# Kernel optimization log

Measured on AMD Instinct MI355X. Metric: run time of the kernel, lower is better.

Reference implementation:

```python
import jax, jax.numpy as jnp
import numpy as np

N_NODES = 100000
N_EDGES = 3200000
HID = 52
N_LAYERS = 3


def setup_inputs() -> dict:
    key = jax.random.key(0)
    ks = jax.random.split(key, 6)
    x = jax.random.normal(ks[0], (N_NODES, HID), dtype=jnp.float32)
    edge_index = jax.random.randint(ks[1], (2, N_EDGES), 0, N_NODES, dtype=jnp.int32)
    w1 = jax.random.normal(ks[2], (N_LAYERS, HID, 2 * HID), dtype=jnp.float32) * 0.1
    b1 = jnp.zeros((N_LAYERS, 2 * HID), dtype=jnp.float32)
    w2 = jax.random.normal(ks[3], (N_LAYERS, 2 * HID, HID), dtype=jnp.float32) * 0.1
    b2 = jnp.zeros((N_LAYERS, HID), dtype=jnp.float32)
    eps = jnp.zeros((N_LAYERS,), dtype=jnp.float32)
    lin_w = jax.random.normal(ks[4], (HID * (N_LAYERS + 1), HID), dtype=jnp.float32) * 0.1
    lin_b = jnp.zeros((HID,), dtype=jnp.float32)
    return {"x": x, "edge_index": edge_index, "w1": w1, "b1": b1,
            "w2": w2, "b2": b2, "eps": eps, "lin_w": lin_w, "lin_b": lin_b}


def reference(x, edge_index, w1, b1, w2, b2, eps, lin_w, lin_b):
    src, dst = edge_index[0], edge_index[1]
    n = x.shape[0]
    h = x
    h_list = [x]
    for l in range(N_LAYERS):
        # GINConv: sum-aggregate neighbor features at target nodes
        agg = jax.ops.segment_sum(h[src], dst, num_segments=n)  # [N, HID]
        z = (1.0 + eps[l]) * h + agg
        # 2-layer MLP: Linear -> ReLU -> Linear
        z = jnp.maximum(z @ w1[l] + b1[l], 0.0) @ w2[l] + b2[l]
        # outer ReLU (dropout p=0 is identity)
        h = jnp.maximum(z, 0.0)
        h_list.append(h)
    node_repr = jnp.concatenate(h_list, axis=1)  # [N, HID*(L+1)]
    return node_repr @ lin_w + lin_b
```

## Files before the change

kernel.cpp:

```cpp
#include <hip/hip_runtime.h>

#define HID 52
#define HID2 104
#define P1_CHUNK 8192
#define NBIN_MAX 512

typedef unsigned short ushort_t;
typedef unsigned int uint_t;
typedef short bf16x8 __attribute__((ext_vector_type(8)));
typedef float f32x4 __attribute__((ext_vector_type(4)));
typedef float f32x2 __attribute__((ext_vector_type(2)));

__device__ __forceinline__ ushort_t f2bf(float f) {
    union { float f; uint_t u; } c; c.f = f;
    uint_t u = c.u + 0x7FFFu + ((c.u >> 16) & 1u);
    return (ushort_t)(u >> 16);
}
__device__ __forceinline__ float bflo(uint_t u) {
    union { uint_t u; float f; } c; c.u = u << 16; return c.f;
}
__device__ __forceinline__ float bfhi(uint_t u) {
    union { uint_t u; float f; } c; c.u = u & 0xFFFF0000u; return c.f;
}
__device__ __forceinline__ f32x2 unpk(uint_t u) {
    return (f32x2){bflo(u), bfhi(u)};
}


__global__ __launch_bounds__(256) void bhist_kernel(const int* __restrict__ dst,
                                                    int* __restrict__ ghist, int E) {
    __shared__ int lh[NBIN_MAX];
    int tid = threadIdx.x;
    lh[tid] = 0; lh[tid + 256] = 0;
    __syncthreads();
    int base = blockIdx.x * P1_CHUNK;
    int cend = min(P1_CHUNK, E - base);
    for (int i = tid; i < cend; i += 256) atomicAdd(&lh[dst[base + i] >> 8], 1);
    __syncthreads();
    int c = lh[tid];       if (c) atomicAdd(&ghist[tid], c);
    c = lh[tid + 256];     if (c) atomicAdd(&ghist[tid + 256], c);
}

__global__ __launch_bounds__(256) void bscan_kernel(const int* __restrict__ ghist,
                                                    int* __restrict__ binstart,
                                                    int* __restrict__ gcur,
                                                    int NBIN, int E) {
    __shared__ int c[NBIN_MAX];
    __shared__ int ps[256];
    int tid = threadIdx.x;
    int b0 = 2 * tid, b1 = 2 * tid + 1;
    c[b0] = ghist[b0]; c[b1] = ghist[b1];
    __syncthreads();
    int pair = c[b0] + c[b1];
    ps[tid] = pair;
    __syncthreads();
    for (int off = 1; off < 256; off <<= 1) {
        int t = (tid >= off) ? ps[tid - off] : 0;
        __syncthreads();
        ps[tid] += t;
        __syncthreads();
    }
    int ex = ps[tid] - pair;
    binstart[b0] = ex;        gcur[b0] = ex;
    binstart[b1] = ex + c[b0]; gcur[b1] = ex + c[b0];
    if (tid == 0) binstart[NBIN] = E;
}

__global__ __launch_bounds__(256) void pass1_kernel(const int* __restrict__ src,
                                                    const int* __restrict__ dst,
                                                    int* __restrict__ gcur,
                                                    uint_t* __restrict__ packed, int E) {
    __shared__ uint_t stage[P1_CHUNK];
    __shared__ ushort_t sbin[P1_CHUNK];
    __shared__ int cnt[NBIN_MAX];
    __shared__ int sst[NBIN_MAX];
    __shared__ int curs[NBIN_MAX];
    __shared__ int gbase[NBIN_MAX];
    __shared__ int ps[256];
    int tid = threadIdx.x;
    int base = blockIdx.x * P1_CHUNK;
    int cend = min(P1_CHUNK, E - base);
    cnt[tid] = 0; cnt[tid + 256] = 0;
    __syncthreads();
    for (int i = tid; i < cend; i += 256) atomicAdd(&cnt[dst[base + i] >> 8], 1);
    __syncthreads();
    int b0 = 2 * tid, b1 = 2 * tid + 1;
    int c0 = cnt[b0], c1 = cnt[b1];
    int pair = c0 + c1;
    ps[tid] = pair;
    __syncthreads();
    for (int off = 1; off < 256; off <<= 1) {
        int t = (tid >= off) ? ps[tid - off] : 0;
        __syncthreads();
        ps[tid] += t;
        __syncthreads();
    }
    int ex = ps[tid] - pair;
    sst[b0] = ex;       curs[b0] = ex;
    sst[b1] = ex + c0;  curs[b1] = ex + c0;
    gbase[b0] = c0 ? atomicAdd(&gcur[b0], c0) : 0;
    gbase[b1] = c1 ? atomicAdd(&gcur[b1], c1) : 0;
    __syncthreads();
    for (int i = tid; i < cend; i += 256) {
        int d = dst[base + i];
        int s = src[base + i];
        int b = d >> 8;
        int pos = atomicAdd(&curs[b], 1);
        stage[pos] = ((uint_t)s << 8) | (uint_t)(d & 255);
        sbin[pos] = (ushort_t)b;
    }
    __syncthreads();
    for (int i = tid; i < cend; i += 256) {
        int b = sbin[i];
        packed[gbase[b] + (i - sst[b])] = stage[i];
    }
}

__global__ __launch_bounds__(256) void pass2_kernel(const uint_t* __restrict__ packed,
                                                    const int* __restrict__ binstart,
                                                    int* __restrict__ srcsorted,
                                                    int* __restrict__ nrs,
                                                    int* __restrict__ ndeg, int N) {
    __shared__ int ncnt[256];
    __shared__ int ps[256];
    __shared__ int curs[256];
    int b = blockIdx.x;
    int beg = binstart[b], end = binstart[b + 1];
    int obase = beg + b * 4096;
    int tid = threadIdx.x;
    ncnt[tid] = 0;
    __syncthreads();
    for (int i = beg + tid; i < end; i += 256) atomicAdd(&ncnt[packed[i] & 255u], 1);
    __syncthreads();
    int v = ncnt[tid];
    int pv = (v + 15) & ~15;
    ps[tid] = pv;
    __syncthreads();
    for (int off = 1; off < 256; off <<= 1) {
        int t = (tid >= off) ? ps[tid - off] : 0;
        __syncthreads();
        ps[tid] += t;
        __syncthreads();
    }
    int start = obase + ps[tid] - pv;
    int node = b * 256 + tid;
    if (node < N) { nrs[node] = start; ndeg[node] = pv; }
    curs[tid] = start;
    __syncthreads();
    for (int i = beg + tid; i < end; i += 256) {
        uint_t p = packed[i];
        int pos = atomicAdd(&curs[p & 255u], 1);
        srcsorted[pos] = (int)(p >> 8);
    }
    __syncthreads();
    for (int i = start + v; i < start + pv; i++) srcsorted[i] = N;
}

__global__ __launch_bounds__(256) void setup_kernel(const float* __restrict__ x,
                                                    const float* __restrict__ w1,
                                                    const float* __restrict__ w2,
                                                    const float* __restrict__ lin_w,
                                                    ushort_t* __restrict__ xb,
                                                    ushort_t* __restrict__ h1b,
                                                    ushort_t* __restrict__ h2b,
                                                    ushort_t* __restrict__ h3b,
                                                    ushort_t* __restrict__ w1f,
                                                    ushort_t* __restrict__ w2f,
                                                    ushort_t* __restrict__ linf,
                                                    int* __restrict__ ghist,
                                                    int n, int nxblk) {
    int blk = blockIdx.x;
    int tid = threadIdx.x;
    if (blk < nxblk) {
        int t = blk * 256 + tid;
        if (t >= n * 16) return;
        int node = t >> 4, pp = t & 15;
        int c0 = pp * 4;
        ushort_t o[4];
#pragma unroll
        for (int j = 0; j < 4; j++) {
            int c = c0 + j;
            o[j] = (c < HID) ? f2bf(x[(size_t)node * HID + c]) : 0;
        }
        uint_t u0 = (uint_t)o[0] | ((uint_t)o[1] << 16);
        uint_t u1 = (uint_t)o[2] | ((uint_t)o[3] << 16);
        *(uint2*)(xb + (size_t)node * 64 + c0) = make_uint2(u0, u1);
        return;
    }
    if (blk == nxblk) {
        ushort_t* arr = (tid < 64) ? xb : (tid < 128) ? h1b : (tid < 192) ? h2b : h3b;
        arr[(size_t)n * 64 + (tid & 63)] = 0;
        ghist[tid] = 0; ghist[tid + 256] = 0;
        return;
    }
    int gid = (blk - nxblk - 1) * 4 + (tid >> 6);
    int lane = tid & 63;
    if (gid >= 122) return;
    int m = lane & 15, q = lane >> 4;
    ushort_t o[8];
    ushort_t* dstp;
    if (gid < 42) {
        int l = gid / 14, r = gid % 14, ct = r >> 1, ks = r & 1;
        int nn = ct * 16 + m;
#pragma unroll
        for (int j = 0; j < 8; j++) {
            int k = ks * 32 + q * 8 + j;
            o[j] = (k < HID && nn < HID2) ? f2bf(w1[((size_t)l * HID + k) * HID2 + nn]) : 0;
        }
        dstp = w1f + ((size_t)(l * 14 + ct * 2 + ks) * 64 + lane) * 8;
    } else if (gid < 90) {
        int g2 = gid - 42, l = g2 / 16, r = g2 % 16, ct = r >> 2, ks = r & 3;
        int nn = ct * 16 + m;
#pragma unroll
        for (int j = 0; j < 8; j++) {
            int k = ks * 32 + q * 8 + j;
            o[j] = (k < HID2 && nn < HID) ? f2bf(w2[((size_t)l * HID2 + k) * HID + nn]) : 0;
        }
        dstp = w2f + ((size_t)(l * 16 + ct * 4 + ks) * 64 + lane) * 8;
    } else {
        int g2 = gid - 90, ct = g2 >> 3, ks = g2 & 7;
        int nn = ct * 16 + m;
#pragma unroll
        for (int j = 0; j < 8; j++) {
            int kg = ks * 32 + q * 8 + j;
            int seg = kg >> 6, kk = kg & 63;
            o[j] = (kk < HID && nn < HID) ? f2bf(lin_w[((size_t)seg * HID + kk) * HID + nn]) : 0;
        }
        dstp = linf + ((size_t)(ct * 8 + ks) * 64 + lane) * 8;
    }
    uint4 u;
    u.x = (uint_t)o[0] | ((uint_t)o[1] << 16);
    u.y = (uint_t)o[2] | ((uint_t)o[3] << 16);
    u.z = (uint_t)o[4] | ((uint_t)o[5] << 16);
    u.w = (uint_t)o[6] | ((uint_t)o[7] << 16);
    *(uint4*)dstp = u;
}

__global__ __launch_bounds__(256) void agg_kernel(const ushort_t* __restrict__ hb,
                                                  const int* __restrict__ nrs,
                                                  const int* __restrict__ ndeg,
                                                  const int* __restrict__ srcsorted,
                                                  const float* __restrict__ eps,
                                                  ushort_t* __restrict__ zb, int n) {
    int wid = (blockIdx.x * blockDim.x + threadIdx.x) >> 6;
    if (wid >= n) return;
    int lane = threadIdx.x & 63;
    int g = lane >> 3, sub = lane & 7;
    int beg = nrs[wid];
    int total = ndeg[wid];
    const ushort_t* hsub = hb + sub * 8;
    const int* ss = srcsorted + beg + g;

    f32x2 A0 = {0,0}, A1 = {0,0}, A2 = {0,0}, A3 = {0,0};
    f32x2 B0 = {0,0}, B1 = {0,0}, B2 = {0,0}, B3 = {0,0};
    if (total > 0) {
        int f0 = ss[0], f1 = ss[8], f2r = ss[16], f3r = ss[24];
        for (int b = 0; b < total; b += 32) {
            bool ok = (b + 16) < total;
            int e0 = f0, e1 = f1;
            int e2 = ok ? f2r : n;
            int e3 = ok ? f3r : n;
            f0 = ss[b + 32]; f1 = ss[b + 40]; f2r = ss[b + 48]; f3r = ss[b + 56];
            uint4 v0 = *(const uint4*)(hsub + (size_t)e0 * 64);
            uint4 v1 = *(const uint4*)(hsub + (size_t)e1 * 64);
            uint4 v2 = *(const uint4*)(hsub + (size_t)e2 * 64);
            uint4 v3 = *(const uint4*)(hsub + (size_t)e3 * 64);
            A0 += unpk(v0.x); A1 += unpk(v0.y); A2 += unpk(v0.z); A3 += unpk(v0.w);
            B0 += unpk(v1.x); B1 += unpk(v1.y); B2 += unpk(v1.z); B3 += unpk(v1.w);
            A0 += unpk(v2.x); A1 += unpk(v2.y); A2 += unpk(v2.z); A3 += unpk(v2.w);
            B0 += unpk(v3.x); B1 += unpk(v3.y); B2 += unpk(v3.z); B3 += unpk(v3.w);
        }
    }
    A0 += B0; A1 += B1; A2 += B2; A3 += B3;
    float a0 = A0.x, a1 = A0.y, a2 = A1.x, a3 = A1.y;
    float a4 = A2.x, a5 = A2.y, a6 = A3.x, a7 = A3.y;
#pragma unroll
    for (int msk = 8; msk <= 32; msk <<= 1) {
        a0 += __shfl_xor(a0, msk); a1 += __shfl_xor(a1, msk);
        a2 += __shfl_xor(a2, msk); a3 += __shfl_xor(a3, msk);
        a4 += __shfl_xor(a4, msk); a5 += __shfl_xor(a5, msk);
        a6 += __shfl_xor(a6, msk); a7 += __shfl_xor(a7, msk);
    }
    if (lane < 8) {
        float sc = 1.0f + eps[0];
        uint4 sv = *(const uint4*)(hb + (size_t)wid * 64 + lane * 8);
        float o0 = fmaf(sc, bflo(sv.x), a0), o1 = fmaf(sc, bfhi(sv.x), a1);
        float o2 = fmaf(sc, bflo(sv.y), a2), o3 = fmaf(sc, bfhi(sv.y), a3);
        float o4 = fmaf(sc, bflo(sv.z), a4), o5 = fmaf(sc, bfhi(sv.z), a5);
        float o6 = fmaf(sc, bflo(sv.w), a6), o7 = fmaf(sc, bfhi(sv.w), a7);
        uint4 u;
        u.x = (uint_t)f2bf(o0) | ((uint_t)f2bf(o1) << 16);
        u.y = (uint_t)f2bf(o2) | ((uint_t)f2bf(o3) << 16);
        u.z = (uint_t)f2bf(o4) | ((uint_t)f2bf(o5) << 16);
        u.w = (uint_t)f2bf(o6) | ((uint_t)f2bf(o7) << 16);
        *(uint4*)(zb + (size_t)wid * 64 + lane * 8) = u;
    }
}

#define HSTRIDE 136
__global__ __launch_bounds__(256) void mlp_kernel(const ushort_t* __restrict__ zb,
                                                  const ushort_t* __restrict__ w1f,
                                                  const float* __restrict__ b1,
                                                  const ushort_t* __restrict__ w2f,
                                                  const float* __restrict__ b2,
                                                  ushort_t* __restrict__ hbout, int n) {
    __shared__ ushort_t hid[64 * HSTRIDE];
    int tid = threadIdx.x;
    int w = tid >> 6, lane = tid & 63, m = lane & 15, q = lane >> 4;
    for (int i = tid; i < 64 * 32; i += 256) {
        int r = i >> 5, c = HID2 + (i & 31);
        hid[r * HSTRIDE + c] = 0;
    }
    __syncthreads();

    int nb = blockIdx.x * 64 + w * 16;
    f32x4 acc1[7];
#pragma unroll
    for (int ct = 0; ct < 7; ct++) {
        int col = ct * 16 + m;
        float bv = (col < HID2) ? b1[col] : 0.f;
        acc1[ct] = (f32x4){bv, bv, bv, bv};
    }
    int anode = min(nb + m, n - 1);
#pragma unroll
    for (int ks = 0; ks < 2; ks++) {
        bf16x8 a = *(const bf16x8*)(zb + (size_t)anode * 64 + ks * 32 + q * 8);
#pragma unroll
        for (int ct = 0; ct < 7; ct++) {
            bf16x8 b = *(const bf16x8*)(w1f + ((size_t)(ct * 2 + ks) * 64 + lane) * 8);
            acc1[ct] = __builtin_amdgcn_mfma_f32_16x16x32_bf16(a, b, acc1[ct], 0, 0, 0);
        }
    }
#pragma unroll
    for (int ct = 0; ct < 7; ct++) {
#pragma unroll
        for (int r = 0; r < 4; r++) {
            float v = fmaxf(acc1[ct][r], 0.f);
            int row = w * 16 + q * 4 + r;
            hid[row * HSTRIDE + ct * 16 + m] = f2bf(v);
        }
    }
    f32x4 acc2[4];
#pragma unroll
    for (int ct = 0; ct < 4; ct++) {
        int col = ct * 16 + m;
        float bv = (col < HID) ? b2[col] : 0.f;
        acc2[ct] = (f32x4){bv, bv, bv, bv};
    }
#pragma unroll
    for (int ks = 0; ks < 4; ks++) {
        bf16x8 a = *(const bf16x8*)&hid[(w * 16 + m) * HSTRIDE + ks * 32 + q * 8];
#pragma unroll
        for (int ct = 0; ct < 4; ct++) {
            bf16x8 b = *(const bf16x8*)(w2f + ((size_t)(ct * 4 + ks) * 64 + lane) * 8);
            acc2[ct] = __builtin_amdgcn_mfma_f32_16x16x32_bf16(a, b, acc2[ct], 0, 0, 0);
        }
    }
#pragma unroll
    for (int ct = 0; ct < 4; ct++) {
#pragma unroll
        for (int r = 0; r < 4; r++) {
            int node = nb + q * 4 + r;
            if (node < n) {
                float v = fmaxf(acc2[ct][r], 0.f);
                hbout[(size_t)node * 64 + ct * 16 + m] = f2bf(v);
            }
        }
    }
}

__global__ __launch_bounds__(256) void final_kernel(const ushort_t* __restrict__ xb,
                                                    const ushort_t* __restrict__ h1b,
                                                    const ushort_t* __restrict__ h2b,
                                                    const ushort_t* __restrict__ h3b,
                                                    const ushort_t* __restrict__ linf,
                                                    const float* __restrict__ lin_b,
                                                    float* __restrict__ out, int ntiles) {
    int tid = threadIdx.x;
    int w = tid >> 6, lane = tid & 63, m = lane & 15, q = lane >> 4;
    int tile = blockIdx.x * 4 + w;
    if (tile >= ntiles) return;
    int nb = tile * 16;
    const ushort_t* segs[4] = {xb, h1b, h2b, h3b};
    f32x4 acc[4];
#pragma unroll
    for (int ct = 0; ct < 4; ct++) {
        int col = ct * 16 + m;
        float bv = (col < HID) ? lin_b[col] : 0.f;
        acc[ct] = (f32x4){bv, bv, bv, bv};
    }
#pragma unroll
    for (int ks = 0; ks < 8; ks++) {
        const ushort_t* p = segs[ks >> 1];
        bf16x8 a = *(const bf16x8*)(p + (size_t)(nb + m) * 64 + (ks & 1) * 32 + q * 8);
#pragma unroll
        for (int ct = 0; ct < 4; ct++) {
            bf16x8 b = *(const bf16x8*)(linf + ((size_t)(ct * 8 + ks) * 64 + lane) * 8);
            acc[ct] = __builtin_amdgcn_mfma_f32_16x16x32_bf16(a, b, acc[ct], 0, 0, 0);
        }
    }
#pragma unroll
    for (int ct = 0; ct < 4; ct++) {
        int col = ct * 16 + m;
        if (col < HID) {
#pragma unroll
            for (int r = 0; r < 4; r++)
                out[(size_t)(nb + q * 4 + r) * HID + col] = acc[ct][r];
        }
    }
}

extern "C" void kernel_launch(void* const* d_in, const int* in_sizes, int n_in,
                              void* d_out, int out_size, void* d_ws, size_t ws_size,
                              hipStream_t stream) {
    const float* x     = (const float*)d_in[0];
    const int*   ei    = (const int*)d_in[1];
    const float* w1    = (const float*)d_in[2];
    const float* b1    = (const float*)d_in[3];
    const float* w2    = (const float*)d_in[4];
    const float* b2    = (const float*)d_in[5];
    const float* eps   = (const float*)d_in[6];
    const float* lin_w = (const float*)d_in[7];
    const float* lin_b = (const float*)d_in[8];
    float* out = (float*)d_out;

    const int N = in_sizes[0] / HID;
    const int E = in_sizes[1] / 2;
    const int* src = ei;
    const int* dst = ei + E;

    const int NBIN = (N + 255) / 256;

    char* p = (char*)d_ws;
    const size_t ROWS = (size_t)(N + 1) * 64 * 2;
    ushort_t* xb  = (ushort_t*)p;  p += ROWS;
    ushort_t* zb  = (ushort_t*)p;  p += ROWS;
    ushort_t* h1b = (ushort_t*)p;  p += ROWS;
    ushort_t* h2b = (ushort_t*)p;  p += ROWS;
    ushort_t* h3b = (ushort_t*)p;  p += ROWS;
    ushort_t* w1f = (ushort_t*)p;  p += 3 * 14 * 512 * 2;
    ushort_t* w2f = (ushort_t*)p;  p += 3 * 16 * 512 * 2;
    ushort_t* linf= (ushort_t*)p;  p += 32 * 512 * 2;
    int* ghist    = (int*)p;       p += 528 * 4;
    int* binstart = (int*)p;       p += 528 * 4;
    int* gcur     = (int*)p;       p += 528 * 4;
    int* nrs      = (int*)p;       p += (size_t)(N + 4) * 4;
    int* ndeg     = (int*)p;       p += (size_t)(N + 4) * 4;
    uint_t* packed = (uint_t*)p;   p += (size_t)E * 4;
    int* srcsorted = (int*)p;

    ushort_t* hbs[4] = {xb, h1b, h2b, h3b};

    const int BLK = 256;
    const int NP1 = (E + P1_CHUNK - 1) / P1_CHUNK;
    const int NXBLK = (N * 16 + BLK - 1) / BLK;
    dim3 blk(BLK);
    dim3 grid_agg(((size_t)N * 64 + BLK - 1) / BLK);

    setup_kernel<<<NXBLK + 1 + 31, blk, 0, stream>>>(x, w1, w2, lin_w,
                                                     xb, h1b, h2b, h3b,
                                                     w1f, w2f, linf, ghist, N, NXBLK);
    bhist_kernel<<<NP1, blk, 0, stream>>>(dst, ghist, E);
    bscan_kernel<<<1, blk, 0, stream>>>(ghist, binstart, gcur, NBIN, E);
    pass1_kernel<<<NP1, blk, 0, stream>>>(src, dst, gcur, packed, E);
    pass2_kernel<<<NBIN, blk, 0, stream>>>(packed, binstart, srcsorted, nrs, ndeg, N);

    const int NBUCK = (N + 63) / 64;
    for (int l = 0; l < 3; l++) {
        agg_kernel<<<grid_agg, blk, 0, stream>>>(hbs[l], nrs, ndeg, srcsorted, eps + l, zb, N);
        mlp_kernel<<<NBUCK, blk, 0, stream>>>(zb,
                                              w1f + (size_t)l * 14 * 512,
                                              b1 + (size_t)l * HID2,
                                              w2f + (size_t)l * 16 * 512,
                                              b2 + (size_t)l * HID,
                                              hbs[l + 1], N);
    }
    final_kernel<<<(6250 + 3) / 4 + 1, blk, 0, stream>>>(xb, h1b, h2b, h3b, linf, lin_b,
                                                         out, (N + 15) / 16);
}
```

Baseline: 403.8 us.

## Fuse neighbor aggregation, MLP, and final projection into one per-layer kernel

Aggregation for each 64-node tile now runs inside the MLP kernel, and the z tile is kept in shared memory instead of going through a global zb buffer. The last layer also fuses the final linear projection, so h3 stays in shared memory. This removes a global round trip of intermediates and four kernel launches. In exchange, each wave now aggregates 16 nodes one after another, which lowers per-node parallelism for the latency-bound gather and raises shared memory use per block, which may reduce occupancy.

```diff
diff --git a/kernel.cpp b/kernel.cpp
--- a/kernel.cpp
+++ b/kernel.cpp
@@ -4,6 +4,7 @@
 #define HID2 104
 #define P1_CHUNK 8192
 #define NBIN_MAX 512
+#define HSTRIDE 136
 
 typedef unsigned short ushort_t;
 typedef unsigned int uint_t;
@@ -163,7 +164,6 @@
                                                     ushort_t* __restrict__ xb,
                                                     ushort_t* __restrict__ h1b,
                                                     ushort_t* __restrict__ h2b,
-                                                    ushort_t* __restrict__ h3b,
                                                     ushort_t* __restrict__ w1f,
                                                     ushort_t* __restrict__ w2f,
                                                     ushort_t* __restrict__ linf,
@@ -188,7 +188,7 @@
         return;
     }
     if (blk == nxblk) {
-        ushort_t* arr = (tid < 64) ? xb : (tid < 128) ? h1b : (tid < 192) ? h2b : h3b;
+        ushort_t* arr = (tid < 64) ? xb : (tid < 128) ? h1b : h2b;
         arr[(size_t)n * 64 + (tid & 63)] = 0;
         ghist[tid] = 0; ghist[tid + 256] = 0;
         return;
@@ -236,84 +236,88 @@
     *(uint4*)dstp = u;
 }
 
-__global__ __launch_bounds__(256) void agg_kernel(const ushort_t* __restrict__ hb,
-                                                  const int* __restrict__ nrs,
-                                                  const int* __restrict__ ndeg,
-                                                  const int* __restrict__ srcsorted,
-                                                  const float* __restrict__ eps,
-                                                  ushort_t* __restrict__ zb, int n) {
-    int wid = (blockIdx.x * blockDim.x + threadIdx.x) >> 6;
-    if (wid >= n) return;
-    int lane = threadIdx.x & 63;
+template<int LAST>
+__global__ __launch_bounds__(256) void layer_kernel(
+        const ushort_t* __restrict__ hbin,
+        const int* __restrict__ nrs, const int* __restrict__ ndeg,
+        const int* __restrict__ srcsorted,
+        const float* __restrict__ eps,
+        const ushort_t* __restrict__ w1f, const float* __restrict__ b1,
+        const ushort_t* __restrict__ w2f, const float* __restrict__ b2,
+        ushort_t* __restrict__ hbout,
+        const ushort_t* __restrict__ xb, const ushort_t* __restrict__ h1b,
+        const ushort_t* __restrict__ linf, const float* __restrict__ lin_b,
+        float* __restrict__ out, int n) {
+    __shared__ uint4 zt[64 * 9];
+    __shared__ ushort_t hid[64 * HSTRIDE];
+    __shared__ ushort_t h3t[LAST ? 64 * 68 : 1];
+
+    int tid = threadIdx.x;
+    int w = tid >> 6, lane = tid & 63;
     int g = lane >> 3, sub = lane & 7;
-    int beg = nrs[wid];
-    int total = ndeg[wid];
-    const ushort_t* hsub = hb + sub * 8;
-    const int* ss = srcsorted + beg + g;
-
-    f32x2 A0 = {0,0}, A1 = {0,0}, A2 = {0,0}, A3 = {0,0};
-    f32x2 B0 = {0,0}, B1 = {0,0}, B2 = {0,0}, B3 = {0,0};
-    if (total > 0) {
-        int f0 = ss[0], f1 = ss[8], f2r = ss[16], f3r = ss[24];
-        for (int b = 0; b < total; b += 32) {
-            bool ok = (b + 16) < total;
-            int e0 = f0, e1 = f1;
-            int e2 = ok ? f2r : n;
-            int e3 = ok ? f3r : n;
-            f0 = ss[b + 32]; f1 = ss[b + 40]; f2r = ss[b + 48]; f3r = ss[b + 56];
-            uint4 v0 = *(const uint4*)(hsub + (size_t)e0 * 64);
-            uint4 v1 = *(const uint4*)(hsub + (size_t)e1 * 64);
-            uint4 v2 = *(const uint4*)(hsub + (size_t)e2 * 64);
-            uint4 v3 = *(const uint4*)(hsub + (size_t)e3 * 64);
-            A0 += unpk(v0.x); A1 += unpk(v0.y); A2 += unpk(v0.z); A3 += unpk(v0.w);
-            B0 += unpk(v1.x); B1 += unpk(v1.y); B2 += unpk(v1.z); B3 += unpk(v1.w);
-            A0 += unpk(v2.x); A1 += unpk(v2.y); A2 += unpk(v2.z); A3 += unpk(v2.w);
-            B0 += unpk(v3.x); B1 += unpk(v3.y); B2 += unpk(v3.z); B3 += unpk(v3.w);
-        }
-    }
-    A0 += B0; A1 += B1; A2 += B2; A3 += B3;
-    float a0 = A0.x, a1 = A0.y, a2 = A1.x, a3 = A1.y;
-    float a4 = A2.x, a5 = A2.y, a6 = A3.x, a7 = A3.y;
-#pragma unroll
-    for (int msk = 8; msk <= 32; msk <<= 1) {
-        a0 += __shfl_xor(a0, msk); a1 += __shfl_xor(a1, msk);
-        a2 += __shfl_xor(a2, msk); a3 += __shfl_xor(a3, msk);
-        a4 += __shfl_xor(a4, msk); a5 += __shfl_xor(a5, msk);
-        a6 += __shfl_xor(a6, msk); a7 += __shfl_xor(a7, msk);
-    }
-    if (lane < 8) {
-        float sc = 1.0f + eps[0];
-        uint4 sv = *(const uint4*)(hb + (size_t)wid * 64 + lane * 8);
-        float o0 = fmaf(sc, bflo(sv.x), a0), o1 = fmaf(sc, bfhi(sv.x), a1);
-        float o2 = fmaf(sc, bflo(sv.y), a2), o3 = fmaf(sc, bfhi(sv.y), a3);
-        float o4 = fmaf(sc, bflo(sv.z), a4), o5 = fmaf(sc, bfhi(sv.z), a5);
-        float o6 = fmaf(sc, bflo(sv.w), a6), o7 = fmaf(sc, bfhi(sv.w), a7);
-        uint4 u;
-        u.x = (uint_t)f2bf(o0) | ((uint_t)f2bf(o1) << 16);
-        u.y = (uint_t)f2bf(o2) | ((uint_t)f2bf(o3) << 16);
-        u.z = (uint_t)f2bf(o4) | ((uint_t)f2bf(o5) << 16);
-        u.w = (uint_t)f2bf(o6) | ((uint_t)f2bf(o7) << 16);
-        *(uint4*)(zb + (size_t)wid * 64 + lane * 8) = u;
-    }
-}
-
-#define HSTRIDE 136
-__global__ __launch_bounds__(256) void mlp_kernel(const ushort_t* __restrict__ zb,
-                                                  const ushort_t* __restrict__ w1f,
-                                                  const float* __restrict__ b1,
-                                                  const ushort_t* __restrict__ w2f,
-                                                  const float* __restrict__ b2,
-                                                  ushort_t* __restrict__ hbout, int n) {
-    __shared__ ushort_t hid[64 * HSTRIDE];
-    int tid = threadIdx.x;
-    int w = tid >> 6, lane = tid & 63, m = lane & 15, q = lane >> 4;
+    int m = lane & 15, q = lane >> 4;
+    int nb = blockIdx.x * 64;
+
     for (int i = tid; i < 64 * 32; i += 256) {
         int r = i >> 5, c = HID2 + (i & 31);
         hid[r * HSTRIDE + c] = 0;
     }
-    __syncthreads();
-
-    int nb = blockIdx.x * 64 + w * 16;
+
+    float sc = 1.0f + eps[0];
+    for (int i = 0; i < 16; i++) {
+        int node = nb + w * 16 + i;
+        int nc = min(node, n - 1);
+        int beg = nrs[nc];
+        int total = ndeg[nc];
+        const ushort_t* hsub = hbin + sub * 8;
+        const int* ss = srcsorted + beg + g;
+
+        f32x2 A0 = {0,0}, A1 = {0,0}, A2 = {0,0}, A3 = {0,0};
+        f32x2 B0 = {0,0}, B1 = {0,0}, B2 = {0,0}, B3 = {0,0};
+        if (total > 0) {
+            int f0 = ss[0], f1 = ss[8], f2r = ss[16], f3r = ss[24];
+            for (int b = 0; b < total; b += 32) {
+                bool ok = (b + 16) < total;
+                int e0 = f0, e1 = f1;
+                int e2 = ok ? f2r : n;
+                int e3 = ok ? f3r : n;
+                f0 = ss[b + 32]; f1 = ss[b + 40]; f2r = ss[b + 48]; f3r = ss[b + 56];
+                uint4 v0 = *(const uint4*)(hsub + (size_t)e0 * 64);
+                uint4 v1 = *(const uint4*)(hsub + (size_t)e1 * 64);
+                uint4 v2 = *(const uint4*)(hsub + (size_t)e2 * 64);
+                uint4 v3 = *(const uint4*)(hsub + (size_t)e3 * 64);
+                A0 += unpk(v0.x); A1 += unpk(v0.y); A2 += unpk(v0.z); A3 += unpk(v0.w);
+                B0 += unpk(v1.x); B1 += unpk(v1.y); B2 += unpk(v1.z); B3 += unpk(v1.w);
+                A0 += unpk(v2.x); A1 += unpk(v2.y); A2 += unpk(v2.z); A3 += unpk(v2.w);
+                B0 += unpk(v3.x); B1 += unpk(v3.y); B2 += unpk(v3.z); B3 += unpk(v3.w);
+            }
+        }
+        A0 += B0; A1 += B1; A2 += B2; A3 += B3;
+        float a0 = A0.x, a1 = A0.y, a2 = A1.x, a3 = A1.y;
+        float a4 = A2.x, a5 = A2.y, a6 = A3.x, a7 = A3.y;
+#pragma unroll
+        for (int msk = 8; msk <= 32; msk <<= 1) {
+            a0 += __shfl_xor(a0, msk); a1 += __shfl_xor(a1, msk);
+            a2 += __shfl_xor(a2, msk); a3 += __shfl_xor(a3, msk);
+            a4 += __shfl_xor(a4, msk); a5 += __shfl_xor(a5, msk);
+            a6 += __shfl_xor(a6, msk); a7 += __shfl_xor(a7, msk);
+        }
+        if (lane < 8) {
+            uint4 sv = *(const uint4*)(hbin + (size_t)nc * 64 + lane * 8);
+            float o0 = fmaf(sc, bflo(sv.x), a0), o1 = fmaf(sc, bfhi(sv.x), a1);
+            float o2 = fmaf(sc, bflo(sv.y), a2), o3 = fmaf(sc, bfhi(sv.y), a3);
+            float o4 = fmaf(sc, bflo(sv.z), a4), o5 = fmaf(sc, bfhi(sv.z), a5);
+            float o6 = fmaf(sc, bflo(sv.w), a6), o7 = fmaf(sc, bfhi(sv.w), a7);
+            uint4 u;
+            u.x = (uint_t)f2bf(o0) | ((uint_t)f2bf(o1) << 16);
+            u.y = (uint_t)f2bf(o2) | ((uint_t)f2bf(o3) << 16);
+            u.z = (uint_t)f2bf(o4) | ((uint_t)f2bf(o5) << 16);
+            u.w = (uint_t)f2bf(o6) | ((uint_t)f2bf(o7) << 16);
+            zt[(w * 16 + i) * 9 + lane] = u;
+        }
+    }
+    __syncthreads();
+
     f32x4 acc1[7];
 #pragma unroll
     for (int ct = 0; ct < 7; ct++) {
@@ -321,10 +325,9 @@
         float bv = (col < HID2) ? b1[col] : 0.f;
         acc1[ct] = (f32x4){bv, bv, bv, bv};
     }
-    int anode = min(nb + m, n - 1);
 #pragma unroll
     for (int ks = 0; ks < 2; ks++) {
-        bf16x8 a = *(const bf16x8*)(zb + (size_t)anode * 64 + ks * 32 + q * 8);
+        bf16x8 a = *(const bf16x8*)&zt[(w * 16 + m) * 9 + ks * 4 + q];
 #pragma unroll
         for (int ct = 0; ct < 7; ct++) {
             bf16x8 b = *(const bf16x8*)(w1f + ((size_t)(ct * 2 + ks) * 64 + lane) * 8);
@@ -356,56 +359,63 @@
             acc2[ct] = __builtin_amdgcn_mfma_f32_16x16x32_bf16(a, b, acc2[ct], 0, 0, 0);
         }
     }
-#pragma unroll
-    for (int ct = 0; ct < 4; ct++) {
-#pragma unroll
-        for (int r = 0; r < 4; r++) {
-            int node = nb + q * 4 + r;
-            if (node < n) {
+
+    if (!LAST) {
+#pragma unroll
+        for (int ct = 0; ct < 4; ct++) {
+#pragma unroll
+            for (int r = 0; r < 4; r++) {
+                int node = nb + w * 16 + q * 4 + r;
+                if (node < n) {
+                    float v = fmaxf(acc2[ct][r], 0.f);
+                    hbout[(size_t)node * 64 + ct * 16 + m] = f2bf(v);
+                }
+            }
+        }
+    } else {
+#pragma unroll
+        for (int ct = 0; ct < 4; ct++) {
+#pragma unroll
+            for (int r = 0; r < 4; r++) {
                 float v = fmaxf(acc2[ct][r], 0.f);
-                hbout[(size_t)node * 64 + ct * 16 + m] = f2bf(v);
-            }
-        }
-    }
-}
-
-__global__ __launch_bounds__(256) void final_kernel(const ushort_t* __restrict__ xb,
-                                                    const ushort_t* __restrict__ h1b,
-                                                    const ushort_t* __restrict__ h2b,
-                                                    const ushort_t* __restrict__ h3b,
-                                                    const ushort_t* __restrict__ linf,
-                                                    const float* __restrict__ lin_b,
-                                                    float* __restrict__ out, int ntiles) {
-    int tid = threadIdx.x;
-    int w = tid >> 6, lane = tid & 63, m = lane & 15, q = lane >> 4;
-    int tile = blockIdx.x * 4 + w;
-    if (tile >= ntiles) return;
-    int nb = tile * 16;
-    const ushort_t* segs[4] = {xb, h1b, h2b, h3b};
-    f32x4 acc[4];
-#pragma unroll
-    for (int ct = 0; ct < 4; ct++) {
-        int col = ct * 16 + m;
-        float bv = (col < HID) ? lin_b[col] : 0.f;
-        acc[ct] = (f32x4){bv, bv, bv, bv};
-    }
-#pragma unroll
-    for (int ks = 0; ks < 8; ks++) {
-        const ushort_t* p = segs[ks >> 1];
-        bf16x8 a = *(const bf16x8*)(p + (size_t)(nb + m) * 64 + (ks & 1) * 32 + q * 8);
+                h3t[(w * 16 + q * 4 + r) * 68 + ct * 16 + m] = f2bf(v);
+            }
+        }
+        f32x4 accF[4];
 #pragma unroll
         for (int ct = 0; ct < 4; ct++) {
-            bf16x8 b = *(const bf16x8*)(linf + ((size_t)(ct * 8 + ks) * 64 + lane) * 8);
-            acc[ct] = __builtin_amdgcn_mfma_f32_16x16x32_bf16(a, b, acc[ct], 0, 0, 0);
-        }
-    }
-#pragma unroll
-    for (int ct = 0; ct < 4; ct++) {
-        int col = ct * 16 + m;
-        if (col < HID) {
-#pragma unroll
-            for (int r = 0; r < 4; r++)
-                out[(size_t)(nb + q * 4 + r) * HID + col] = acc[ct][r];
+            int col = ct * 16 + m;
+            float bv = (col < HID) ? lin_b[col] : 0.f;
+            accF[ct] = (f32x4){bv, bv, bv, bv};
+        }
+        int nodeA = min(nb + w * 16 + m, n - 1);
+        const ushort_t* segs[3] = {xb, h1b, hbin};
+#pragma unroll
+        for (int ks = 0; ks < 8; ks++) {
+            bf16x8 a;
+            if (ks < 6) {
+                const ushort_t* p = segs[ks >> 1];
+                a = *(const bf16x8*)(p + (size_t)nodeA * 64 + (ks & 1) * 32 + q * 8);
+            } else {
+                a = *(const bf16x8*)&h3t[(w * 16 + m) * 68 + (ks & 1) * 32 + q * 8];
+            }
+#pragma unroll
+            for (int ct = 0; ct < 4; ct++) {
+                bf16x8 b = *(const bf16x8*)(linf + ((size_t)(ct * 8 + ks) * 64 + lane) * 8);
+                accF[ct] = __builtin_amdgcn_mfma_f32_16x16x32_bf16(a, b, accF[ct], 0, 0, 0);
+            }
+        }
+#pragma unroll
+        for (int ct = 0; ct < 4; ct++) {
+            int col = ct * 16 + m;
+            if (col < HID) {
+#pragma unroll
+                for (int r = 0; r < 4; r++) {
+                    int node = nb + w * 16 + q * 4 + r;
+                    if (node < n)
+                        out[(size_t)node * HID + col] = accF[ct][r];
+                }
+            }
         }
     }
 }
@@ -434,10 +444,8 @@
     char* p = (char*)d_ws;
     const size_t ROWS = (size_t)(N + 1) * 64 * 2;
     ushort_t* xb  = (ushort_t*)p;  p += ROWS;
-    ushort_t* zb  = (ushort_t*)p;  p += ROWS;
     ushort_t* h1b = (ushort_t*)p;  p += ROWS;
     ushort_t* h2b = (ushort_t*)p;  p += ROWS;
-    ushort_t* h3b = (ushort_t*)p;  p += ROWS;
     ushort_t* w1f = (ushort_t*)p;  p += 3 * 14 * 512 * 2;
     ushort_t* w2f = (ushort_t*)p;  p += 3 * 16 * 512 * 2;
     ushort_t* linf= (ushort_t*)p;  p += 32 * 512 * 2;
@@ -449,32 +457,33 @@
     uint_t* packed = (uint_t*)p;   p += (size_t)E * 4;
     int* srcsorted = (int*)p;
 
-    ushort_t* hbs[4] = {xb, h1b, h2b, h3b};
-
     const int BLK = 256;
     const int NP1 = (E + P1_CHUNK - 1) / P1_CHUNK;
     const int NXBLK = (N * 16 + BLK - 1) / BLK;
+    const int NBUCK = (N + 63) / 64;
     dim3 blk(BLK);
-    dim3 grid_agg(((size_t)N * 64 + BLK - 1) / BLK);
 
     setup_kernel<<<NXBLK + 1 + 31, blk, 0, stream>>>(x, w1, w2, lin_w,
-                                                     xb, h1b, h2b, h3b,
+                                                     xb, h1b, h2b,
                                                      w1f, w2f, linf, ghist, N, NXBLK);
     bhist_kernel<<<NP1, blk, 0, stream>>>(dst, ghist, E);
     bscan_kernel<<<1, blk, 0, stream>>>(ghist, binstart, gcur, NBIN, E);
     pass1_kernel<<<NP1, blk, 0, stream>>>(src, dst, gcur, packed, E);
     pass2_kernel<<<NBIN, blk, 0, stream>>>(packed, binstart, srcsorted, nrs, ndeg, N);
 
-    const int NBUCK = (N + 63) / 64;
-    for (int l = 0; l < 3; l++) {
-        agg_kernel<<<grid_agg, blk, 0, stream>>>(hbs[l], nrs, ndeg, srcsorted, eps + l, zb, N);
-        mlp_kernel<<<NBUCK, blk, 0, stream>>>(zb,
-                                              w1f + (size_t)l * 14 * 512,
-                                              b1 + (size_t)l * HID2,
-                                              w2f + (size_t)l * 16 * 512,
-                                              b2 + (size_t)l * HID,
-                                              hbs[l + 1], N);
-    }
-    final_kernel<<<(6250 + 3) / 4 + 1, blk, 0, stream>>>(xb, h1b, h2b, h3b, linf, lin_b,
-                                                         out, (N + 15) / 16);
-}
+    layer_kernel<0><<<NBUCK, blk, 0, stream>>>(xb, nrs, ndeg, srcsorted, eps + 0,
+                                               w1f + 0 * 14 * 512, b1 + 0 * HID2,
+                                               w2f + 0 * 16 * 512, b2 + 0 * HID,
+                                               h1b, nullptr, nullptr, nullptr, nullptr,
+                                               nullptr, N);
+    layer_kernel<0><<<NBUCK, blk, 0, stream>>>(h1b, nrs, ndeg, srcsorted, eps + 1,
+                                               w1f + 1 * 14 * 512, b1 + 1 * HID2,
+                                               w2f + 1 * 16 * 512, b2 + 1 * HID,
+                                               h2b, nullptr, nullptr, nullptr, nullptr,
+                                               nullptr, N);
+    layer_kernel<1><<<NBUCK, blk, 0, stream>>>(h2b, nrs, ndeg, srcsorted, eps + 2,
+                                               w1f + 2 * 14 * 512, b1 + 2 * HID2,
+                                               w2f + 2 * 16 * 512, b2 + 2 * HID,
+                                               nullptr, xb, h1b,
+                                               linf, lin_b, out, N);
+}
```

Result: slower. 464.7 us (+15.1%).

## Fuse bin histogram into setup kernel and drop separate scan kernel

Applied to the files above, without the earlier changes.

The destination-bin histogram moves into extra blocks of the setup kernel, and the standalone scan kernel is removed. pass1 and pass2 now each recompute the bin prefix sum from the global histogram, and a memset zeroes the counters. pass2 also sub-sorts each node's edge list by the high bit of the source index, so gathers in the aggregation kernel get some locality. This trades two kernel launches for redundant per-block scans, and it adds a larger shared-memory histogram in pass2.

```diff
diff --git a/kernel.cpp b/kernel.cpp
--- a/kernel.cpp
+++ b/kernel.cpp
@@ -4,6 +4,7 @@
 #define HID2 104
 #define P1_CHUNK 8192
 #define NBIN_MAX 512
+#define HSTRIDE 136
 
 typedef unsigned short ushort_t;
 typedef unsigned int uint_t;
@@ -26,140 +27,11 @@
     return (f32x2){bflo(u), bfhi(u)};
 }
 
-
-__global__ __launch_bounds__(256) void bhist_kernel(const int* __restrict__ dst,
-                                                    int* __restrict__ ghist, int E) {
-    __shared__ int lh[NBIN_MAX];
-    int tid = threadIdx.x;
-    lh[tid] = 0; lh[tid + 256] = 0;
-    __syncthreads();
-    int base = blockIdx.x * P1_CHUNK;
-    int cend = min(P1_CHUNK, E - base);
-    for (int i = tid; i < cend; i += 256) atomicAdd(&lh[dst[base + i] >> 8], 1);
-    __syncthreads();
-    int c = lh[tid];       if (c) atomicAdd(&ghist[tid], c);
-    c = lh[tid + 256];     if (c) atomicAdd(&ghist[tid + 256], c);
-}
-
-__global__ __launch_bounds__(256) void bscan_kernel(const int* __restrict__ ghist,
-                                                    int* __restrict__ binstart,
-                                                    int* __restrict__ gcur,
-                                                    int NBIN, int E) {
-    __shared__ int c[NBIN_MAX];
-    __shared__ int ps[256];
-    int tid = threadIdx.x;
-    int b0 = 2 * tid, b1 = 2 * tid + 1;
-    c[b0] = ghist[b0]; c[b1] = ghist[b1];
-    __syncthreads();
-    int pair = c[b0] + c[b1];
-    ps[tid] = pair;
-    __syncthreads();
-    for (int off = 1; off < 256; off <<= 1) {
-        int t = (tid >= off) ? ps[tid - off] : 0;
-        __syncthreads();
-        ps[tid] += t;
-        __syncthreads();
-    }
-    int ex = ps[tid] - pair;
-    binstart[b0] = ex;        gcur[b0] = ex;
-    binstart[b1] = ex + c[b0]; gcur[b1] = ex + c[b0];
-    if (tid == 0) binstart[NBIN] = E;
-}
-
-__global__ __launch_bounds__(256) void pass1_kernel(const int* __restrict__ src,
-                                                    const int* __restrict__ dst,
-                                                    int* __restrict__ gcur,
-                                                    uint_t* __restrict__ packed, int E) {
-    __shared__ uint_t stage[P1_CHUNK];
-    __shared__ ushort_t sbin[P1_CHUNK];
-    __shared__ int cnt[NBIN_MAX];
-    __shared__ int sst[NBIN_MAX];
-    __shared__ int curs[NBIN_MAX];
-    __shared__ int gbase[NBIN_MAX];
-    __shared__ int ps[256];
-    int tid = threadIdx.x;
-    int base = blockIdx.x * P1_CHUNK;
-    int cend = min(P1_CHUNK, E - base);
-    cnt[tid] = 0; cnt[tid + 256] = 0;
-    __syncthreads();
-    for (int i = tid; i < cend; i += 256) atomicAdd(&cnt[dst[base + i] >> 8], 1);
-    __syncthreads();
-    int b0 = 2 * tid, b1 = 2 * tid + 1;
-    int c0 = cnt[b0], c1 = cnt[b1];
-    int pair = c0 + c1;
-    ps[tid] = pair;
-    __syncthreads();
-    for (int off = 1; off < 256; off <<= 1) {
-        int t = (tid >= off) ? ps[tid - off] : 0;
-        __syncthreads();
-        ps[tid] += t;
-        __syncthreads();
-    }
-    int ex = ps[tid] - pair;
-    sst[b0] = ex;       curs[b0] = ex;
-    sst[b1] = ex + c0;  curs[b1] = ex + c0;
-    gbase[b0] = c0 ? atomicAdd(&gcur[b0], c0) : 0;
-    gbase[b1] = c1 ? atomicAdd(&gcur[b1], c1) : 0;
-    __syncthreads();
-    for (int i = tid; i < cend; i += 256) {
-        int d = dst[base + i];
-        int s = src[base + i];
-        int b = d >> 8;
-        int pos = atomicAdd(&curs[b], 1);
-        stage[pos] = ((uint_t)s << 8) | (uint_t)(d & 255);
-        sbin[pos] = (ushort_t)b;
-    }
-    __syncthreads();
-    for (int i = tid; i < cend; i += 256) {
-        int b = sbin[i];
-        packed[gbase[b] + (i - sst[b])] = stage[i];
-    }
-}
-
-__global__ __launch_bounds__(256) void pass2_kernel(const uint_t* __restrict__ packed,
-                                                    const int* __restrict__ binstart,
-                                                    int* __restrict__ srcsorted,
-                                                    int* __restrict__ nrs,
-                                                    int* __restrict__ ndeg, int N) {
-    __shared__ int ncnt[256];
-    __shared__ int ps[256];
-    __shared__ int curs[256];
-    int b = blockIdx.x;
-    int beg = binstart[b], end = binstart[b + 1];
-    int obase = beg + b * 4096;
-    int tid = threadIdx.x;
-    ncnt[tid] = 0;
-    __syncthreads();
-    for (int i = beg + tid; i < end; i += 256) atomicAdd(&ncnt[packed[i] & 255u], 1);
-    __syncthreads();
-    int v = ncnt[tid];
-    int pv = (v + 15) & ~15;
-    ps[tid] = pv;
-    __syncthreads();
-    for (int off = 1; off < 256; off <<= 1) {
-        int t = (tid >= off) ? ps[tid - off] : 0;
-        __syncthreads();
-        ps[tid] += t;
-        __syncthreads();
-    }
-    int start = obase + ps[tid] - pv;
-    int node = b * 256 + tid;
-    if (node < N) { nrs[node] = start; ndeg[node] = pv; }
-    curs[tid] = start;
-    __syncthreads();
-    for (int i = beg + tid; i < end; i += 256) {
-        uint_t p = packed[i];
-        int pos = atomicAdd(&curs[p & 255u], 1);
-        srcsorted[pos] = (int)(p >> 8);
-    }
-    __syncthreads();
-    for (int i = start + v; i < start + pv; i++) srcsorted[i] = N;
-}
-
 __global__ __launch_bounds__(256) void setup_kernel(const float* __restrict__ x,
                                                     const float* __restrict__ w1,
                                                     const float* __restrict__ w2,
                                                     const float* __restrict__ lin_w,
+                                                    const int* __restrict__ dst,
                                                     ushort_t* __restrict__ xb,
                                                     ushort_t* __restrict__ h1b,
                                                     ushort_t* __restrict__ h2b,
@@ -168,7 +40,8 @@
                                                     ushort_t* __restrict__ w2f,
                                                     ushort_t* __restrict__ linf,
                                                     int* __restrict__ ghist,
-                                                    int n, int nxblk) {
+                                                    int n, int E, int nxblk) {
+    __shared__ int lh[NBIN_MAX];
     int blk = blockIdx.x;
     int tid = threadIdx.x;
     if (blk < nxblk) {
@@ -190,50 +63,197 @@
     if (blk == nxblk) {
         ushort_t* arr = (tid < 64) ? xb : (tid < 128) ? h1b : (tid < 192) ? h2b : h3b;
         arr[(size_t)n * 64 + (tid & 63)] = 0;
-        ghist[tid] = 0; ghist[tid + 256] = 0;
         return;
     }
-    int gid = (blk - nxblk - 1) * 4 + (tid >> 6);
-    int lane = tid & 63;
-    if (gid >= 122) return;
-    int m = lane & 15, q = lane >> 4;
-    ushort_t o[8];
-    ushort_t* dstp;
-    if (gid < 42) {
-        int l = gid / 14, r = gid % 14, ct = r >> 1, ks = r & 1;
-        int nn = ct * 16 + m;
-#pragma unroll
-        for (int j = 0; j < 8; j++) {
-            int k = ks * 32 + q * 8 + j;
-            o[j] = (k < HID && nn < HID2) ? f2bf(w1[((size_t)l * HID + k) * HID2 + nn]) : 0;
-        }
-        dstp = w1f + ((size_t)(l * 14 + ct * 2 + ks) * 64 + lane) * 8;
-    } else if (gid < 90) {
-        int g2 = gid - 42, l = g2 / 16, r = g2 % 16, ct = r >> 2, ks = r & 3;
-        int nn = ct * 16 + m;
-#pragma unroll
-        for (int j = 0; j < 8; j++) {
-            int k = ks * 32 + q * 8 + j;
-            o[j] = (k < HID2 && nn < HID) ? f2bf(w2[((size_t)l * HID2 + k) * HID + nn]) : 0;
-        }
-        dstp = w2f + ((size_t)(l * 16 + ct * 4 + ks) * 64 + lane) * 8;
-    } else {
-        int g2 = gid - 90, ct = g2 >> 3, ks = g2 & 7;
-        int nn = ct * 16 + m;
-#pragma unroll
-        for (int j = 0; j < 8; j++) {
-            int kg = ks * 32 + q * 8 + j;
-            int seg = kg >> 6, kk = kg & 63;
-            o[j] = (kk < HID && nn < HID) ? f2bf(lin_w[((size_t)seg * HID + kk) * HID + nn]) : 0;
-        }
-        dstp = linf + ((size_t)(ct * 8 + ks) * 64 + lane) * 8;
-    }
-    uint4 u;
-    u.x = (uint_t)o[0] | ((uint_t)o[1] << 16);
-    u.y = (uint_t)o[2] | ((uint_t)o[3] << 16);
-    u.z = (uint_t)o[4] | ((uint_t)o[5] << 16);
-    u.w = (uint_t)o[6] | ((uint_t)o[7] << 16);
-    *(uint4*)dstp = u;
+    if (blk < nxblk + 32) {
+        int gid = (blk - nxblk - 1) * 4 + (tid >> 6);
+        int lane = tid & 63;
+        if (gid >= 122) return;
+        int m = lane & 15, q = lane >> 4;
+        ushort_t o[8];
+        ushort_t* dstp;
+        if (gid < 42) {
+            int l = gid / 14, r = gid % 14, ct = r >> 1, ks = r & 1;
+            int nn = ct * 16 + m;
+#pragma unroll
+            for (int j = 0; j < 8; j++) {
+                int k = ks * 32 + q * 8 + j;
+                o[j] = (k < HID && nn < HID2) ? f2bf(w1[((size_t)l * HID + k) * HID2 + nn]) : 0;
+            }
+            dstp = w1f + ((size_t)(l * 14 + ct * 2 + ks) * 64 + lane) * 8;
+        } else if (gid < 90) {
+            int g2 = gid - 42, l = g2 / 16, r = g2 % 16, ct = r >> 2, ks = r & 3;
+            int nn = ct * 16 + m;
+#pragma unroll
+            for (int j = 0; j < 8; j++) {
+                int k = ks * 32 + q * 8 + j;
+                o[j] = (k < HID2 && nn < HID) ? f2bf(w2[((size_t)l * HID2 + k) * HID + nn]) : 0;
+            }
+            dstp = w2f + ((size_t)(l * 16 + ct * 4 + ks) * 64 + lane) * 8;
+        } else {
+            int g2 = gid - 90, ct = g2 >> 3, ks = g2 & 7;
+            int nn = ct * 16 + m;
+#pragma unroll
+            for (int j = 0; j < 8; j++) {
+                int kg = ks * 32 + q * 8 + j;
+                int seg = kg >> 6, kk = kg & 63;
+                o[j] = (kk < HID && nn < HID) ? f2bf(lin_w[((size_t)seg * HID + kk) * HID + nn]) : 0;
+            }
+            dstp = linf + ((size_t)(ct * 8 + ks) * 64 + lane) * 8;
+        }
+        uint4 u;
+        u.x = (uint_t)o[0] | ((uint_t)o[1] << 16);
+        u.y = (uint_t)o[2] | ((uint_t)o[3] << 16);
+        u.z = (uint_t)o[4] | ((uint_t)o[5] << 16);
+        u.w = (uint_t)o[6] | ((uint_t)o[7] << 16);
+        *(uint4*)dstp = u;
+        return;
+    }
+    int eblk = blk - nxblk - 32;
+    lh[tid] = 0; lh[tid + 256] = 0;
+    __syncthreads();
+    int base = eblk * P1_CHUNK;
+    int cend = min(P1_CHUNK, E - base);
+    for (int i = tid; i < cend; i += 256) atomicAdd(&lh[dst[base + i] >> 8], 1);
+    __syncthreads();
+    int cc = lh[tid];       if (cc) atomicAdd(&ghist[tid], cc);
+    cc = lh[tid + 256];     if (cc) atomicAdd(&ghist[tid + 256], cc);
+}
+
+__global__ __launch_bounds__(256) void pass1_kernel(const int* __restrict__ src,
+                                                    const int* __restrict__ dst,
+                                                    const int* __restrict__ ghist,
+                                                    int* __restrict__ gcnt,
+                                                    uint_t* __restrict__ packed, int E) {
+    __shared__ uint_t stage[P1_CHUNK];
+    __shared__ ushort_t sbin[P1_CHUNK];
+    __shared__ int gh[NBIN_MAX];
+    __shared__ int cnt[NBIN_MAX];
+    __shared__ int sst[NBIN_MAX];
+    __shared__ int curs[NBIN_MAX];
+    __shared__ int gbase[NBIN_MAX];
+    __shared__ int ps[256];
+    int tid = threadIdx.x;
+    int b0 = 2 * tid, b1 = 2 * tid + 1;
+    gh[b0] = ghist[b0]; gh[b1] = ghist[b1];
+    cnt[tid] = 0; cnt[tid + 256] = 0;
+    __syncthreads();
+    int gpair = gh[b0] + gh[b1];
+    ps[tid] = gpair;
+    __syncthreads();
+    for (int off = 1; off < 256; off <<= 1) {
+        int t = (tid >= off) ? ps[tid - off] : 0;
+        __syncthreads();
+        ps[tid] += t;
+        __syncthreads();
+    }
+    int bst0 = ps[tid] - gpair;
+    int bst1 = bst0 + gh[b0];
+    __syncthreads();
+    int base = blockIdx.x * P1_CHUNK;
+    int cend = min(P1_CHUNK, E - base);
+    for (int i = tid; i < cend; i += 256) atomicAdd(&cnt[dst[base + i] >> 8], 1);
+    __syncthreads();
+    int c0 = cnt[b0], c1 = cnt[b1];
+    int pair = c0 + c1;
+    ps[tid] = pair;
+    __syncthreads();
+    for (int off = 1; off < 256; off <<= 1) {
+        int t = (tid >= off) ? ps[tid - off] : 0;
+        __syncthreads();
+        ps[tid] += t;
+        __syncthreads();
+    }
+    int ex = ps[tid] - pair;
+    sst[b0] = ex;       curs[b0] = ex;
+    sst[b1] = ex + c0;  curs[b1] = ex + c0;
+    gbase[b0] = c0 ? (bst0 + atomicAdd(&gcnt[b0], c0)) : 0;
+    gbase[b1] = c1 ? (bst1 + atomicAdd(&gcnt[b1], c1)) : 0;
+    __syncthreads();
+    for (int i = tid; i < cend; i += 256) {
+        int d = dst[base + i];
+        int s = src[base + i];
+        int b = d >> 8;
+        int pos = atomicAdd(&curs[b], 1);
+        stage[pos] = ((uint_t)s << 8) | (uint_t)(d & 255);
+        sbin[pos] = (ushort_t)b;
+    }
+    __syncthreads();
+    for (int i = tid; i < cend; i += 256) {
+        int b = sbin[i];
+        packed[gbase[b] + (i - sst[b])] = stage[i];
+    }
+}
+
+__global__ __launch_bounds__(256) void pass2_kernel(const uint_t* __restrict__ packed,
+                                                    const int* __restrict__ ghist,
+                                                    int* __restrict__ srcsorted,
+                                                    int* __restrict__ nrs,
+                                                    int* __restrict__ ndeg, int N) {
+    __shared__ int c[NBIN_MAX];
+    __shared__ int ps[256];
+    __shared__ int hist[1024];
+    __shared__ int curs[1024];
+    int b = blockIdx.x;
+    int tid = threadIdx.x;
+    int b0 = 2 * tid, b1 = 2 * tid + 1;
+    c[b0] = ghist[b0]; c[b1] = ghist[b1];
+    hist[tid] = 0; hist[tid + 256] = 0; hist[tid + 512] = 0; hist[tid + 768] = 0;
+    __syncthreads();
+    int gpair = c[b0] + c[b1];
+    ps[tid] = gpair;
+    __syncthreads();
+    for (int off = 1; off < 256; off <<= 1) {
+        int t = (tid >= off) ? ps[tid - off] : 0;
+        __syncthreads();
+        ps[tid] += t;
+        __syncthreads();
+    }
+    int e0 = ps[tid] - gpair;
+    int cntb0 = c[b0], cntb1 = c[b1];
+    __syncthreads();
+    c[b0] = e0;
+    c[b1] = e0 + cntb0;
+    __syncthreads();
+    int beg = c[b];
+    int cntb = (b == b0) ? cntb0 : 0;
+    cntb = ghist[b];
+    int end = beg + cntb;
+    int obase = beg + b * 4096;
+    for (int i = beg + tid; i < end; i += 256) {
+        uint_t p = packed[i];
+        int key = ((int)(p & 255u) << 2) | (int)((p >> 8) >> 15);
+        atomicAdd(&hist[key], 1);
+    }
+    __syncthreads();
+    int h0 = hist[tid * 4], h1 = hist[tid * 4 + 1], h2 = hist[tid * 4 + 2], h3 = hist[tid * 4 + 3];
+    int v = h0 + h1 + h2 + h3;
+    int pv = (v + 15) & ~15;
+    ps[tid] = pv;
+    __syncthreads();
+    for (int off = 1; off < 256; off <<= 1) {
+        int t = (tid >= off) ? ps[tid - off] : 0;
+        __syncthreads();
+        ps[tid] += t;
+        __syncthreads();
+    }
+    int start = obase + ps[tid] - pv;
+    int node = b * 256 + tid;
+    if (node < N) { nrs[node] = start; ndeg[node] = pv; }
+    curs[tid * 4 + 0] = start;
+    curs[tid * 4 + 1] = start + h0;
+    curs[tid * 4 + 2] = start + h0 + h1;
+    curs[tid * 4 + 3] = start + h0 + h1 + h2;
+    __syncthreads();
+    for (int i = beg + tid; i < end; i += 256) {
+        uint_t p = packed[i];
+        int s = (int)(p >> 8);
+        int key = ((int)(p & 255u) << 2) | (s >> 15);
+        int pos = atomicAdd(&curs[key], 1);
+        srcsorted[pos] = s;
+    }
+    __syncthreads();
+    for (int i = start + v; i < start + pv; i++) srcsorted[i] = N;
 }
 
 __global__ __launch_bounds__(256) void agg_kernel(const ushort_t* __restrict__ hb,
@@ -297,7 +317,6 @@
     }
 }
 
-#define HSTRIDE 136
 __global__ __launch_bounds__(256) void mlp_kernel(const ushort_t* __restrict__ zb,
                                                   const ushort_t* __restrict__ w1f,
                                                   const float* __restrict__ b1,
@@ -441,9 +460,8 @@
     ushort_t* w1f = (ushort_t*)p;  p += 3 * 14 * 512 * 2;
     ushort_t* w2f = (ushort_t*)p;  p += 3 * 16 * 512 * 2;
     ushort_t* linf= (ushort_t*)p;  p += 32 * 512 * 2;
-    int* ghist    = (int*)p;       p += 528 * 4;
-    int* binstart = (int*)p;       p += 528 * 4;
-    int* gcur     = (int*)p;       p += 528 * 4;
+    int* ghist    = (int*)p;       p += 512 * 4;
+    int* gcnt     = (int*)p;       p += 512 * 4;
     int* nrs      = (int*)p;       p += (size_t)(N + 4) * 4;
     int* ndeg     = (int*)p;       p += (size_t)(N + 4) * 4;
     uint_t* packed = (uint_t*)p;   p += (size_t)E * 4;
@@ -454,18 +472,17 @@
     const int BLK = 256;
     const int NP1 = (E + P1_CHUNK - 1) / P1_CHUNK;
     const int NXBLK = (N * 16 + BLK - 1) / BLK;
+    const int NBUCK = (N + 63) / 64;
     dim3 blk(BLK);
     dim3 grid_agg(((size_t)N * 64 + BLK - 1) / BLK);
 
-    setup_kernel<<<NXBLK + 1 + 31, blk, 0, stream>>>(x, w1, w2, lin_w,
-                                                     xb, h1b, h2b, h3b,
-                                                     w1f, w2f, linf, ghist, N, NXBLK);
-    bhist_kernel<<<NP1, blk, 0, stream>>>(dst, ghist, E);
-    bscan_kernel<<<1, blk, 0, stream>>>(ghist, binstart, gcur, NBIN, E);
-    pass1_kernel<<<NP1, blk, 0, stream>>>(src, dst, gcur, packed, E);
-    pass2_kernel<<<NBIN, blk, 0, stream>>>(packed, binstart, srcsorted, nrs, ndeg, N);
-
-    const int NBUCK = (N + 63) / 64;
+    hipMemsetAsync(ghist, 0, 1024 * sizeof(int), stream);
+    setup_kernel<<<NXBLK + 32 + NP1, blk, 0, stream>>>(x, w1, w2, lin_w, dst,
+                                                       xb, h1b, h2b, h3b,
+                                                       w1f, w2f, linf, ghist, N, E, NXBLK);
+    pass1_kernel<<<NP1, blk, 0, stream>>>(src, dst, ghist, gcnt, packed, E);
+    pass2_kernel<<<NBIN, blk, 0, stream>>>(packed, ghist, srcsorted, nrs, ndeg, N);
+
     for (int l = 0; l < 3; l++) {
         agg_kernel<<<grid_agg, blk, 0, stream>>>(hbs[l], nrs, ndeg, srcsorted, eps + l, zb, N);
         mlp_kernel<<<NBUCK, blk, 0, stream>>>(zb,
```

Result: no change. 407.3 us (+0.9%).
